# Kernel tuning notes

Hardware: AMD Instinct MI355X
Metric: run time of the kernel (lower is better)

## Reference

```python
import jax, jax.numpy as jnp
import numpy as np

DIM = 768
HEADS = 12
HEAD_DIM = DIM // HEADS
SCALE = HEAD_DIM ** (-0.5)


def setup_inputs() -> dict:
    key = jax.random.key(0)
    k1, k2, k3, k4 = jax.random.split(key, 4)
    B, N = 2, 48 * 48
    x = jax.random.normal(k1, (B, N, DIM), dtype=jnp.float32)
    qkv_w = jax.random.normal(k2, (3 * DIM, DIM), dtype=jnp.float32) * (DIM ** -0.5)
    proj_w = jax.random.normal(k3, (DIM, DIM), dtype=jnp.float32) * (DIM ** -0.5)
    proj_b = jax.random.normal(k4, (DIM,), dtype=jnp.float32) * 0.02
    return {"x": x, "H": 48, "W": 48, "qkv_w": qkv_w, "proj_w": proj_w, "proj_b": proj_b}


def reference(x, H, W, qkv_w, proj_w, proj_b):
    B, N, C = x.shape
    h, d = HEADS, HEAD_DIM
    # qkv linear (no bias): [B,N,3C], then split into per-head q,k,v [B,h,N,d]
    qkv = jnp.einsum('bnc,fc->bnf', x, qkv_w)
    qkv = qkv.reshape(B, N, 3, h, d).transpose(2, 0, 3, 1, 4)
    q, k, v = qkv[0], qkv[1], qkv[2]
    attn = jnp.einsum('bhnd,bhmd->bhnm', q, k) * SCALE  # [B,h,N,N]
    attn = jax.nn.softmax(attn, axis=-1)
    out = jnp.einsum('bhnm,bhmd->bhnd', attn, v)  # [B,h,N,d]
    out = out.transpose(0, 2, 1, 3).reshape(B, N, C)
    out = jnp.einsum('bnc,fc->bnf', out, proj_w) + proj_b
    return out
```

## Files before the change

kernel.cpp:

```cpp
#include <hip/hip_runtime.h>

#define B_    2
#define N_    2304
#define C_    768
#define HEADS 12
#define D_    64
#define F3    2304
#define M_    (B_*N_)
#define SPLITS 2
#define KSPAN (N_/SPLITS)
#define QSCALE 0.18033688011112042f

typedef __attribute__((ext_vector_type(8)))  short bfrag;
typedef __attribute__((ext_vector_type(4)))  float ffrag;
typedef __attribute__((ext_vector_type(16))) float ffrag16;
typedef __attribute__((ext_vector_type(4)))  unsigned ufrag;

__device__ __forceinline__ short f2bf(float f) {
    unsigned u = __float_as_uint(f);
    u += 0x7fff + ((u >> 16) & 1);
    return (short)(u >> 16);
}

__device__ __forceinline__ void gl2lds16(const void* g, void* l) {
    __builtin_amdgcn_global_load_lds(
        (const __attribute__((address_space(1))) void*)g,
        (__attribute__((address_space(3))) void*)l, 16, 0, 0);
}

__device__ __forceinline__ unsigned pktrunc(float a, float b) {
    return __builtin_amdgcn_perm(__float_as_uint(a), __float_as_uint(b),
                                 0x03020706u);
}

__global__ __launch_bounds__(256) void cast_all(const float* __restrict__ x,
                                                const float* __restrict__ qw,
                                                const float* __restrict__ pw,
                                                short* __restrict__ dst) {
    const int nx4 = (M_*C_)/4, nq4 = (F3*C_)/4, np4 = (C_*C_)/4;
    int i = blockIdx.x * 256 + threadIdx.x;
    if (i >= nx4 + nq4 + np4) return;
    const float* src; int off;
    if (i < nx4)            { src = x;  off = i; }
    else if (i < nx4 + nq4) { src = qw; off = i - nx4; }
    else                    { src = pw; off = i - nx4 - nq4; }
    float4 v = ((const float4*)src)[off];
    short4 o;
    o.x = f2bf(v.x); o.y = f2bf(v.y); o.z = f2bf(v.z); o.w = f2bf(v.w);
    ((short4*)dst)[i] = o;
}

__global__ __launch_bounds__(256) void qkv_gemm(const short* __restrict__ xb,
                                                const short* __restrict__ wb,
                                                short* __restrict__ Qb,
                                                short* __restrict__ Kb,
                                                short* __restrict__ Vtb) {
    __shared__ short As[128*32];
    __shared__ short Bs[128*32];
    const int t = threadIdx.x;
    const int w = t >> 6, lane = t & 63;
    const int quad = lane >> 4, l15 = lane & 15;
    const int wr = w >> 1, wc = w & 1;
    const int m0 = blockIdx.y * 128, f0 = blockIdx.x * 128;

    ffrag acc[4][4] = {};

    for (int k0 = 0; k0 < C_; k0 += 32) {
        __syncthreads();
        #pragma unroll
        for (int r = 0; r < 2; ++r) {
            int seg = r*4 + w;
            int row = seg*16 + (lane >> 2);
            int kk  = (lane & 3) * 8;
            gl2lds16(xb + (size_t)(m0+row)*C_ + k0 + kk, As + seg*512);
            gl2lds16(wb + (size_t)(f0+row)*C_ + k0 + kk, Bs + seg*512);
        }
        __syncthreads();
        bfrag af[4], bf[4];
        #pragma unroll
        for (int i = 0; i < 4; ++i)
            af[i] = *(const bfrag*)(As + (wr*64 + i*16 + l15)*32 + quad*8);
        #pragma unroll
        for (int j = 0; j < 4; ++j)
            bf[j] = *(const bfrag*)(Bs + (wc*64 + j*16 + l15)*32 + quad*8);
        #pragma unroll
        for (int i = 0; i < 4; ++i)
            #pragma unroll
            for (int j = 0; j < 4; ++j)
                acc[i][j] = __builtin_amdgcn_mfma_f32_16x16x32_bf16(af[i], bf[j], acc[i][j], 0, 0, 0);
    }

    const int b   = m0 / N_;
    const int seg = f0 + wc*64;
    const int which = seg / C_;
    const int head  = (seg - which*C_) >> 6;
    const int bh    = b*HEADS + head;
    const int nbase = (m0 - b*N_) + wr*64 + quad*4;

    if (which == 0) {
        #pragma unroll
        for (int i = 0; i < 4; ++i) {
            int n0 = nbase + i*16;
            #pragma unroll
            for (int j = 0; j < 4; ++j) {
                int d = j*16 + l15;
                #pragma unroll
                for (int r = 0; r < 4; ++r)
                    Qb[((size_t)bh*N_ + n0 + r)*D_ + d] = f2bf(acc[i][j][r] * QSCALE);
            }
        }
    } else if (which == 1) {
        #pragma unroll
        for (int i = 0; i < 4; ++i) {
            int n0 = nbase + i*16;
            #pragma unroll
            for (int j = 0; j < 4; ++j) {
                int d = j*16 + l15;
                #pragma unroll
                for (int r = 0; r < 4; ++r)
                    Kb[((size_t)bh*N_ + n0 + r)*D_ + d] = f2bf(acc[i][j][r]);
            }
        }
    } else {
        #pragma unroll
        for (int i = 0; i < 4; ++i) {
            int n0 = nbase + i*16;
            #pragma unroll
            for (int j = 0; j < 4; ++j) {
                int d = j*16 + l15;
                short4 vv;
                vv.x = f2bf(acc[i][j][0]);
                vv.y = f2bf(acc[i][j][1]);
                vv.z = f2bf(acc[i][j][2]);
                vv.w = f2bf(acc[i][j][3]);
                *(short4*)(Vtb + ((size_t)bh*D_ + d)*N_ + n0) = vv;
            }
        }
    }
}

__global__ __launch_bounds__(128) void attn_mfma(const short* __restrict__ Qb,
                                                 const short* __restrict__ Kb,
                                                 const short* __restrict__ Vtb,
                                                 float* __restrict__ Opart,
                                                 float* __restrict__ lpart) {
    __shared__ short Qs[64*64];
    __shared__ short Ks[64*64];
    __shared__ short Vts[64*64];
    const int t = threadIdx.x;
    const int w = t >> 6, lane = t & 63;
    const int l31 = lane & 31, hi = lane >> 5;
    const int bh = blockIdx.x, q0 = blockIdx.y * 64;
    const int split = blockIdx.z;
    const int kbase = split * KSPAN;
    const size_t base = (size_t)bh * N_ * D_;
    const int lrow = lane >> 3;
    const int lc   = (lane & 7) ^ lrow;

    #pragma unroll
    for (int r = 0; r < 4; ++r) {
        int s = r*2 + w;
        int row = s*8 + lrow;
        gl2lds16(Qb + base + (size_t)(q0+row)*D_ + lc*8, Qs + s*512);
    }
    __syncthreads();

    bfrag qf[4];
    {
        int row = w*32 + l31, r7 = row & 7;
        #pragma unroll
        for (int kc = 0; kc < 4; ++kc)
            qf[kc] = *(const bfrag*)(Qs + row*64 + ((kc*2 + hi) ^ r7)*8);
    }

    bfrag vones;
    #pragma unroll
    for (int j = 0; j < 8; ++j) vones[j] = (short)0x3f80;

    ffrag16 oacc[2], lfr;
    #pragma unroll
    for (int r = 0; r < 16; ++r) { oacc[0][r] = 0.f; oacc[1][r] = 0.f; lfr[r] = 0.f; }

    for (int k0 = kbase; k0 < kbase + KSPAN; k0 += 64) {
        __syncthreads();
        #pragma unroll
        for (int r = 0; r < 4; ++r) {
            int s = r*2 + w;
            int row = s*8 + lrow;
            gl2lds16(Kb  + base + (size_t)(k0+row)*D_ + lc*8,    Ks  + s*512);
            gl2lds16(Vtb + (size_t)(bh*D_ + row)*N_ + k0 + lc*8, Vts + s*512);
        }
        __syncthreads();

        ufrag pfr[4];
        #pragma unroll
        for (int kt = 0; kt < 2; ++kt) {
            ffrag16 s;
            #pragma unroll
            for (int r = 0; r < 16; ++r) s[r] = 0.f;
            int row = kt*32 + l31, r7 = row & 7;
            #pragma unroll
            for (int kc = 0; kc < 4; ++kc) {
                bfrag kf = *(const bfrag*)(Ks + row*64 + ((kc*2 + hi) ^ r7)*8);
                s = __builtin_amdgcn_mfma_f32_32x32x16_bf16(kf, qf[kc], s, 0, 0, 0);
            }
            #pragma unroll
            for (int r = 0; r < 16; ++r)
                s[r] = __builtin_amdgcn_exp2f(s[r]);
            unsigned q01_0 = pktrunc(s[0],  s[1]),  q23_0 = pktrunc(s[2],  s[3]);
            unsigned q01_1 = pktrunc(s[4],  s[5]),  q23_1 = pktrunc(s[6],  s[7]);
            unsigned q01_2 = pktrunc(s[8],  s[9]),  q23_2 = pktrunc(s[10], s[11]);
            unsigned q01_3 = pktrunc(s[12], s[13]), q23_3 = pktrunc(s[14], s[15]);
            unsigned r0 = __shfl_xor(hi ? q01_0 : q01_1, 32, 64);
            unsigned r1 = __shfl_xor(hi ? q23_0 : q23_1, 32, 64);
            unsigned r2 = __shfl_xor(hi ? q01_2 : q01_3, 32, 64);
            unsigned r3 = __shfl_xor(hi ? q23_2 : q23_3, 32, 64);
            ufrag lo, hif;
            lo[0] = hi ? r0 : q01_0;  lo[1] = hi ? r1 : q23_0;
            lo[2] = hi ? q01_1 : r0;  lo[3] = hi ? q23_1 : r1;
            hif[0] = hi ? r2 : q01_2; hif[1] = hi ? r3 : q23_2;
            hif[2] = hi ? q01_3 : r2; hif[3] = hi ? q23_3 : r3;
            pfr[kt*2]     = lo;
            pfr[kt*2 + 1] = hif;
        }

        #pragma unroll
        for (int kc = 0; kc < 4; ++kc) {
            bfrag pf = __builtin_bit_cast(bfrag, pfr[kc]);
            #pragma unroll
            for (int dt = 0; dt < 2; ++dt) {
                int row = dt*32 + l31, r7 = row & 7;
                bfrag vf = *(const bfrag*)(Vts + row*64 + ((kc*2 + hi) ^ r7)*8);
                oacc[dt] = __builtin_amdgcn_mfma_f32_32x32x16_bf16(pf, vf, oacc[dt], 0, 0, 0);
            }
            lfr = __builtin_amdgcn_mfma_f32_32x32x16_bf16(pf, vones, lfr, 0, 0, 0);
        }
    }

    const int b = bh / HEADS, head = bh - b*HEADS;
    float* Op = Opart + (size_t)split * M_ * C_;
    float* lp = lpart + (size_t)split * (B_*HEADS) * N_;

    if (l31 == 0) {
        #pragma unroll
        for (int r = 0; r < 16; ++r) {
            int n = q0 + w*32 + (r & 3) + 8*(r >> 2) + 4*hi;
            lp[bh*N_ + n] = lfr[r];
        }
    }

    #pragma unroll
    for (int dt = 0; dt < 2; ++dt)
        #pragma unroll
        for (int r = 0; r < 16; ++r) {
            int n = q0 + w*32 + (r & 3) + 8*(r >> 2) + 4*hi;
            int c = head*D_ + dt*32 + l31;
            Op[((size_t)b*N_ + n)*C_ + c] = oacc[dt][r];
        }
}

__global__ __launch_bounds__(256) void attn_merge(const float* __restrict__ Opart,
                                                  const float* __restrict__ lpart,
                                                  short* __restrict__ Ob) {
    int i = blockIdx.x * 256 + threadIdx.x;
    int m = i / (C_/4);
    int c = (i - m*(C_/4)) * 4;
    int b = m / N_, n = m - b*N_;
    int bh = b*HEADS + (c >> 6);
    float4 o0 = ((const float4*)Opart)[i];
    float4 o1 = ((const float4*)(Opart + (size_t)M_*C_))[i];
    float l = lpart[bh*N_ + n] + lpart[(B_*HEADS)*N_ + bh*N_ + n];
    float inv = 1.f / l;
    short4 o;
    o.x = f2bf((o0.x + o1.x) * inv);
    o.y = f2bf((o0.y + o1.y) * inv);
    o.z = f2bf((o0.z + o1.z) * inv);
    o.w = f2bf((o0.w + o1.w) * inv);
    ((short4*)Ob)[i] = o;
}

__global__ __launch_bounds__(256) void proj_gemm(const short* __restrict__ Ab,
                                                 const short* __restrict__ wb,
                                                 const float* __restrict__ bias,
                                                 float* __restrict__ out) {
    __shared__ short As[128*32];
    __shared__ short Bs[128*32];
    const int t = threadIdx.x;
    const int w = t >> 6, lane = t & 63;
    const int quad = lane >> 4, l15 = lane & 15;
    const int wr = w >> 1, wc = w & 1;
    const int m0 = blockIdx.y * 128, f0 = blockIdx.x * 128;

    ffrag acc[4][4] = {};

    for (int k0 = 0; k0 < C_; k0 += 32) {
        __syncthreads();
        #pragma unroll
        for (int r = 0; r < 2; ++r) {
            int seg = r*4 + w;
            int row = seg*16 + (lane >> 2);
            int kk  = (lane & 3) * 8;
            gl2lds16(Ab + (size_t)(m0+row)*C_ + k0 + kk, As + seg*512);
            gl2lds16(wb + (size_t)(f0+row)*C_ + k0 + kk, Bs + seg*512);
        }
        __syncthreads();
        bfrag af[4], bf[4];
        #pragma unroll
        for (int i = 0; i < 4; ++i)
            af[i] = *(const bfrag*)(As + (wr*64 + i*16 + l15)*32 + quad*8);
        #pragma unroll
        for (int j = 0; j < 4; ++j)
            bf[j] = *(const bfrag*)(Bs + (wc*64 + j*16 + l15)*32 + quad*8);
        #pragma unroll
        for (int i = 0; i < 4; ++i)
            #pragma unroll
            for (int j = 0; j < 4; ++j)
                acc[i][j] = __builtin_amdgcn_mfma_f32_16x16x32_bf16(af[i], bf[j], acc[i][j], 0, 0, 0);
    }

    #pragma unroll
    for (int i = 0; i < 4; ++i) {
        int mbase = m0 + wr*64 + i*16 + quad*4;
        #pragma unroll
        for (int j = 0; j < 4; ++j) {
            int f = f0 + wc*64 + j*16 + l15;
            float bv = bias[f];
            #pragma unroll
            for (int r = 0; r < 4; ++r)
                out[(size_t)(mbase + r)*C_ + f] = acc[i][j][r] + bv;
        }
    }
}

extern "C" void kernel_launch(void* const* d_in, const int* in_sizes, int n_in,
                              void* d_out, int out_size, void* d_ws, size_t ws_size,
                              hipStream_t stream) {
    const float* x      = (const float*)d_in[0];
    const float* qkv_w  = (const float*)d_in[3];
    const float* proj_w = (const float*)d_in[4];
    const float* proj_b = (const float*)d_in[5];
    float* out = (float*)d_out;

    const size_t nx = (size_t)M_ * C_;
    const size_t nq = (size_t)F3 * C_;
    const size_t np = (size_t)C_ * C_;
    short* xb  = (short*)d_ws;
    short* qwb = xb  + nx;
    short* pwb = qwb + nq;
    short* Qb  = pwb + np;
    short* Kb  = Qb  + nx;
    short* Vtb = Kb  + nx;
    short* Ob  = Vtb + nx;
    float* Opart = (float*)(Ob + nx);
    float* lpart = Opart + (size_t)SPLITS * M_ * C_;

    const int ncast4 = (int)((nx + nq + np) / 4);
    cast_all<<<dim3((ncast4 + 255)/256), 256, 0, stream>>>(x, qkv_w, proj_w, xb);

    qkv_gemm<<<dim3(F3/128, M_/128), 256, 0, stream>>>(xb, qwb, Qb, Kb, Vtb);
    attn_mfma<<<dim3(B_*HEADS, N_/64, SPLITS), 128, 0, stream>>>(Qb, Kb, Vtb, Opart, lpart);
    attn_merge<<<dim3(((int)(nx/4) + 255)/256), 256, 0, stream>>>(Opart, lpart, Ob);
    proj_gemm<<<dim3(C_/128, M_/128), 256, 0, stream>>>(Ob, pwb, proj_b, out);
}
```

Before: 213.6 us.

## Double-buffer K/V tiles in attention with 4-wave blocks and permlane swaps

The attention kernel now uses 256-thread blocks that each cover 128 query rows. K/V tiles are double-buffered in shared memory, so the next tile's global-to-LDS load is issued while the current tile is computed, which cuts the two barriers per iteration down to one. It also raises wave priority around the MFMA sections and replaces the shfl_xor and select sequence with permlane32_swap for the P-fragment exchange. In exchange, shared memory use per block rises, the Q buffer aliases the second K/V buffer (safe only because of the added barrier), and there are fewer, larger blocks.

```diff
diff --git a/kernel.cpp b/kernel.cpp
--- a/kernel.cpp
+++ b/kernel.cpp
@@ -15,6 +15,7 @@
 typedef __attribute__((ext_vector_type(4)))  float ffrag;
 typedef __attribute__((ext_vector_type(16))) float ffrag16;
 typedef __attribute__((ext_vector_type(4)))  unsigned ufrag;
+typedef __attribute__((ext_vector_type(2)))  unsigned uint2v;
 
 __device__ __forceinline__ short f2bf(float f) {
     unsigned u = __float_as_uint(f);
@@ -139,29 +140,35 @@
     }
 }
 
-__global__ __launch_bounds__(128) void attn_mfma(const short* __restrict__ Qb,
-                                                 const short* __restrict__ Kb,
-                                                 const short* __restrict__ Vtb,
-                                                 float* __restrict__ Opart,
-                                                 float* __restrict__ lpart) {
-    __shared__ short Qs[64*64];
-    __shared__ short Ks[64*64];
-    __shared__ short Vts[64*64];
+__global__ __launch_bounds__(256, 4) void attn_mfma(const short* __restrict__ Qb,
+                                                    const short* __restrict__ Kb,
+                                                    const short* __restrict__ Vtb,
+                                                    float* __restrict__ Opart,
+                                                    float* __restrict__ lpart) {
+    __shared__ short lds[16384];
     const int t = threadIdx.x;
     const int w = t >> 6, lane = t & 63;
     const int l31 = lane & 31, hi = lane >> 5;
-    const int bh = blockIdx.x, q0 = blockIdx.y * 64;
+    const int bh = blockIdx.x, q0 = blockIdx.y * 128;
     const int split = blockIdx.z;
     const int kbase = split * KSPAN;
     const size_t base = (size_t)bh * N_ * D_;
     const int lrow = lane >> 3;
     const int lc   = (lane & 7) ^ lrow;
 
+    short* Qs = lds + 8192;
+
     #pragma unroll
     for (int r = 0; r < 4; ++r) {
-        int s = r*2 + w;
+        int s = r*4 + w;
+        gl2lds16(Qb + base + (size_t)(q0 + s*8 + lrow)*D_ + lc*8, Qs + s*512);
+    }
+    #pragma unroll
+    for (int r = 0; r < 2; ++r) {
+        int s = r*4 + w;
         int row = s*8 + lrow;
-        gl2lds16(Qb + base + (size_t)(q0+row)*D_ + lc*8, Qs + s*512);
+        gl2lds16(Kb  + base + (size_t)(kbase+row)*D_ + lc*8,    lds + s*512);
+        gl2lds16(Vtb + (size_t)(bh*D_ + row)*N_ + kbase + lc*8, lds + 4096 + s*512);
     }
     __syncthreads();
 
@@ -172,6 +179,7 @@
         for (int kc = 0; kc < 4; ++kc)
             qf[kc] = *(const bfrag*)(Qs + row*64 + ((kc*2 + hi) ^ r7)*8);
     }
+    __syncthreads();
 
     bfrag vones;
     #pragma unroll
@@ -181,16 +189,23 @@
     #pragma unroll
     for (int r = 0; r < 16; ++r) { oacc[0][r] = 0.f; oacc[1][r] = 0.f; lfr[r] = 0.f; }
 
-    for (int k0 = kbase; k0 < kbase + KSPAN; k0 += 64) {
-        __syncthreads();
-        #pragma unroll
-        for (int r = 0; r < 4; ++r) {
-            int s = r*2 + w;
-            int row = s*8 + lrow;
-            gl2lds16(Kb  + base + (size_t)(k0+row)*D_ + lc*8,    Ks  + s*512);
-            gl2lds16(Vtb + (size_t)(bh*D_ + row)*N_ + k0 + lc*8, Vts + s*512);
-        }
-        __syncthreads();
+    const int NT = KSPAN / 64;
+    for (int ti = 0; ti < NT; ++ti) {
+        const int cur = ti & 1;
+        const short* Kc = lds + cur*8192;
+        const short* Vc = Kc + 4096;
+
+        if (ti + 1 < NT) {
+            short* Kn = lds + (cur^1)*8192;
+            const int k0n = kbase + (ti+1)*64;
+            #pragma unroll
+            for (int r = 0; r < 2; ++r) {
+                int s = r*4 + w;
+                int row = s*8 + lrow;
+                gl2lds16(Kb  + base + (size_t)(k0n+row)*D_ + lc*8,    Kn + s*512);
+                gl2lds16(Vtb + (size_t)(bh*D_ + row)*N_ + k0n + lc*8, Kn + 4096 + s*512);
+            }
+        }
 
         ufrag pfr[4];
         #pragma unroll
@@ -199,11 +214,13 @@
             #pragma unroll
             for (int r = 0; r < 16; ++r) s[r] = 0.f;
             int row = kt*32 + l31, r7 = row & 7;
+            __builtin_amdgcn_s_setprio(1);
             #pragma unroll
             for (int kc = 0; kc < 4; ++kc) {
-                bfrag kf = *(const bfrag*)(Ks + row*64 + ((kc*2 + hi) ^ r7)*8);
+                bfrag kf = *(const bfrag*)(Kc + row*64 + ((kc*2 + hi) ^ r7)*8);
                 s = __builtin_amdgcn_mfma_f32_32x32x16_bf16(kf, qf[kc], s, 0, 0, 0);
             }
+            __builtin_amdgcn_s_setprio(0);
             #pragma unroll
             for (int r = 0; r < 16; ++r)
                 s[r] = __builtin_amdgcn_exp2f(s[r]);
@@ -211,30 +228,31 @@
             unsigned q01_1 = pktrunc(s[4],  s[5]),  q23_1 = pktrunc(s[6],  s[7]);
             unsigned q01_2 = pktrunc(s[8],  s[9]),  q23_2 = pktrunc(s[10], s[11]);
             unsigned q01_3 = pktrunc(s[12], s[13]), q23_3 = pktrunc(s[14], s[15]);
-            unsigned r0 = __shfl_xor(hi ? q01_0 : q01_1, 32, 64);
-            unsigned r1 = __shfl_xor(hi ? q23_0 : q23_1, 32, 64);
-            unsigned r2 = __shfl_xor(hi ? q01_2 : q01_3, 32, 64);
-            unsigned r3 = __shfl_xor(hi ? q23_2 : q23_3, 32, 64);
+            uint2v e0 = __builtin_amdgcn_permlane32_swap(q01_0, q01_1, false, false);
+            uint2v e1 = __builtin_amdgcn_permlane32_swap(q23_0, q23_1, false, false);
+            uint2v e2 = __builtin_amdgcn_permlane32_swap(q01_2, q01_3, false, false);
+            uint2v e3 = __builtin_amdgcn_permlane32_swap(q23_2, q23_3, false, false);
             ufrag lo, hif;
-            lo[0] = hi ? r0 : q01_0;  lo[1] = hi ? r1 : q23_0;
-            lo[2] = hi ? q01_1 : r0;  lo[3] = hi ? q23_1 : r1;
-            hif[0] = hi ? r2 : q01_2; hif[1] = hi ? r3 : q23_2;
-            hif[2] = hi ? q01_3 : r2; hif[3] = hi ? q23_3 : r3;
+            lo[0]  = e0[0]; lo[1]  = e1[0]; lo[2]  = e0[1]; lo[3]  = e1[1];
+            hif[0] = e2[0]; hif[1] = e3[0]; hif[2] = e2[1]; hif[3] = e3[1];
             pfr[kt*2]     = lo;
             pfr[kt*2 + 1] = hif;
         }
 
+        __builtin_amdgcn_s_setprio(1);
         #pragma unroll
         for (int kc = 0; kc < 4; ++kc) {
             bfrag pf = __builtin_bit_cast(bfrag, pfr[kc]);
             #pragma unroll
             for (int dt = 0; dt < 2; ++dt) {
                 int row = dt*32 + l31, r7 = row & 7;
-                bfrag vf = *(const bfrag*)(Vts + row*64 + ((kc*2 + hi) ^ r7)*8);
+                bfrag vf = *(const bfrag*)(Vc + row*64 + ((kc*2 + hi) ^ r7)*8);
                 oacc[dt] = __builtin_amdgcn_mfma_f32_32x32x16_bf16(pf, vf, oacc[dt], 0, 0, 0);
             }
             lfr = __builtin_amdgcn_mfma_f32_32x32x16_bf16(pf, vones, lfr, 0, 0, 0);
         }
+        __builtin_amdgcn_s_setprio(0);
+        __syncthreads();
     }
 
     const int b = bh / HEADS, head = bh - b*HEADS;
@@ -358,7 +376,7 @@
     cast_all<<<dim3((ncast4 + 255)/256), 256, 0, stream>>>(x, qkv_w, proj_w, xb);
 
     qkv_gemm<<<dim3(F3/128, M_/128), 256, 0, stream>>>(xb, qwb, Qb, Kb, Vtb);
-    attn_mfma<<<dim3(B_*HEADS, N_/64, SPLITS), 128, 0, stream>>>(Qb, Kb, Vtb, Opart, lpart);
+    attn_mfma<<<dim3(B_*HEADS, N_/128, SPLITS), 256, 0, stream>>>(Qb, Kb, Vtb, Opart, lpart);
     attn_merge<<<dim3(((int)(nx/4) + 255)/256), 256, 0, stream>>>(Opart, lpart, Ob);
     proj_gemm<<<dim3(C_/128, M_/128), 256, 0, stream>>>(Ob, pwb, proj_b, out);
 }
```

New measurement: 197.7 us. -7.4%, faster.
